# Kernel tuning notes

Hardware: AMD Instinct MI355X
Metric: run time of the kernel (lower is better)

The kernel has to match this reference:

```python
import jax, jax.numpy as jnp
import numpy as np

N = 50000      # nodes
E = 800000     # edges (avg degree 16)
F_IN = 256     # num_node_features
H = 256        # hidden_dim
L = 2          # num_message_passing_rounds - 1 hidden conv layers


def setup_inputs() -> dict:
    key = jax.random.key(0)
    ks = jax.random.split(key, 8)
    x = jax.random.normal(ks[0], (N, F_IN), dtype=jnp.float32)
    edge_index = jax.random.randint(ks[1], (2, E), 0, N, dtype=jnp.int32)
    init = lambda k, shape, fan: jax.random.normal(k, shape, dtype=jnp.float32) / np.float32(np.sqrt(fan))
    WA_in = init(ks[2], (F_IN, H), F_IN)   # proj_in.A weight (stored [in,out])
    WB_in = init(ks[3], (F_IN, H), F_IN)   # proj_in.B weight
    A_stack = init(ks[4], (L, H, H), H)    # conv layers' A weights
    B_stack = init(ks[5], (L, H, H), H)    # conv layers' B weights
    W_out = init(ks[6], (H, 1), H)         # proj_out weight
    b_out = jnp.zeros((1,), jnp.float32)   # proj_out bias
    return {"x": x, "edge_index": edge_index, "WA_in": WA_in, "WB_in": WB_in,
            "A_stack": A_stack, "B_stack": B_stack, "W_out": W_out, "b_out": b_out}


def reference(x, edge_index, WA_in, WB_in, A_stack, B_stack, W_out, b_out):
    src, dst = edge_index[0], edge_index[1]
    # in-degree per node; PyG scatter-mean divides by max(deg, 1)
    deg = jax.ops.segment_sum(jnp.ones((E,), x.dtype), dst, num_segments=N)
    inv_deg = (1.0 / jnp.maximum(deg, 1.0))[:, None]  # [N,1]

    def mean_agg(h):
        # gather x_j = h[src], scatter-mean into dst -> [N, d]
        return jax.ops.segment_sum(h[src], dst, num_segments=N) * inv_deg

    # proj_in: A(mean_msg) + B(x)
    h = mean_agg(x) @ WA_in + x @ WB_in
    # hidden conv rounds with sigmoid (use_relu=False)
    for i in range(L):
        h = jax.nn.sigmoid(mean_agg(h) @ A_stack[i] + h @ B_stack[i])
    # proj_out + squeeze (output_logits=True)
    return (h @ W_out + b_out).squeeze()  # [N]
```

## Files before the change

### kernel.cpp

```cpp
#include <hip/hip_runtime.h>

typedef unsigned short u16;
typedef unsigned int u32;
typedef __attribute__((ext_vector_type(8))) short short8;
typedef __attribute__((ext_vector_type(4))) float f32x4;
typedef __attribute__((ext_vector_type(2))) float f32x2;

__device__ __forceinline__ float bf2f(u16 u) {
    return __uint_as_float(((u32)u) << 16);
}
__device__ __forceinline__ u16 f2bf(float f) {
    u32 u = __float_as_uint(f);
    u += 0x7fff + ((u >> 16) & 1);
    return (u16)(u >> 16);
}
__device__ __forceinline__ u32 pack2(float a, float b) {
    return (u32)f2bf(a) | ((u32)f2bf(b) << 16);
}
__device__ __forceinline__ u32 pk_fp8x4(float f0, float f1, float f2, float f3) {
    int w = __builtin_amdgcn_cvt_pk_fp8_f32(f0, f1, 0, false);
    w = __builtin_amdgcn_cvt_pk_fp8_f32(f2, f3, w, true);
    return (u32)w;
}
__device__ __forceinline__ void acc4(float* a, u32 w) {
    f32x2 lo = __builtin_amdgcn_cvt_pk_f32_fp8((int)w, false);
    f32x2 hi = __builtin_amdgcn_cvt_pk_f32_fp8((int)w, true);
    a[0] += lo.x; a[1] += lo.y; a[2] += hi.x; a[3] += hi.y;
}
__device__ __forceinline__ void acc4m(float* a, u32 w, float m) {
    f32x2 lo = __builtin_amdgcn_cvt_pk_f32_fp8((int)w, false);
    f32x2 hi = __builtin_amdgcn_cvt_pk_f32_fp8((int)w, true);
    a[0] += m * lo.x; a[1] += m * lo.y; a[2] += m * hi.x; a[3] += m * hi.y;
}
__device__ __forceinline__ void acc16(float* a, uint4 v) {
    acc4(a + 0, v.x); acc4(a + 4, v.y); acc4(a + 8, v.z); acc4(a + 12, v.w);
}
__device__ __forceinline__ void acc16m(float* a, uint4 v, float m) {
    acc4m(a + 0, v.x, m); acc4m(a + 4, v.y, m); acc4m(a + 8, v.z, m); acc4m(a + 12, v.w, m);
}


__global__ void cvt_x_kernel(const float* __restrict__ x, u16* __restrict__ xb,
                             u32* __restrict__ xq, int n) {
    int i = blockIdx.x * 256 + threadIdx.x;
    int row = i >> 6;
    ushort4 o;
    u32 q;
    if (row < n) {
        float4 v = ((const float4*)x)[i];
        o.x = f2bf(v.x); o.y = f2bf(v.y); o.z = f2bf(v.z); o.w = f2bf(v.w);
        q = pk_fp8x4(v.x, v.y, v.z, v.w);
    } else {
        o.x = o.y = o.z = o.w = 0;
        q = 0;
    }
    ((ushort4*)xb)[i] = o;
    xq[i] = q;
}

__global__ void cvt_h_kernel(const u16* __restrict__ hb, uint2* __restrict__ hq, int ngroups) {
    int j = blockIdx.x * 256 + threadIdx.x;
    if (j >= ngroups) return;
    uint4 v = ((const uint4*)hb)[j];
    float f0 = bf2f(v.x & 0xffff), f1 = bf2f(v.x >> 16);
    float f2 = bf2f(v.y & 0xffff), f3 = bf2f(v.y >> 16);
    float f4 = bf2f(v.z & 0xffff), f5 = bf2f(v.z >> 16);
    float f6 = bf2f(v.w & 0xffff), f7 = bf2f(v.w >> 16);
    uint2 o;
    o.x = pk_fp8x4(f0, f1, f2, f3);
    o.y = pk_fp8x4(f4, f5, f6, f7);
    hq[j] = o;
}

__global__ void cvt_w_kernel(const float* __restrict__ WA, const float* __restrict__ WB,
                             const float* __restrict__ As, const float* __restrict__ Bs,
                             u16* __restrict__ wT, int nlayers) {
    int i = blockIdx.x * 256 + threadIdx.x;
    const int per = 256 * 512;
    if (i >= nlayers * per) return;
    int l = i / per;
    int rem = i - l * per;
    int nn = rem >> 9;
    int k = rem & 511;
    const float* Aw = (l == 0) ? WA : As + (size_t)(l - 1) * 65536;
    const float* Bw = (l == 0) ? WB : Bs + (size_t)(l - 1) * 65536;
    float v = (k < 256) ? Aw[(size_t)k * 256 + nn] : Bw[(size_t)(k - 256) * 256 + nn];
    wT[i] = f2bf(v);
}


__global__ __launch_bounds__(256) void hist_kernel(const int* __restrict__ dst,
                                                   int* __restrict__ ccnt, int e, int nb) {
    __shared__ int h[256];
    int tid = threadIdx.x;
    h[tid] = 0;
    __syncthreads();
    int e0 = blockIdx.x * 4096;
#pragma unroll
    for (int j = 0; j < 16; ++j) {
        int i = e0 + j * 256 + tid;
        if (i < e) atomicAdd(&h[dst[i] >> 8], 1);
    }
    __syncthreads();
    if (tid < nb) {
        int v = h[tid];
        if (v) atomicAdd(&ccnt[tid], v);
    }
}

__global__ __launch_bounds__(256) void scan_coarse_kernel(const int* __restrict__ ccnt,
                                                          int* __restrict__ cbase,
                                                          int* __restrict__ rowptr,
                                                          int nb, int n, int e) {
    __shared__ int sh[256];
    int t = threadIdx.x;
    int v = (t < nb) ? ccnt[t] : 0;
    int x = v;
    sh[t] = x; __syncthreads();
    for (int o = 1; o < 256; o <<= 1) {
        int y = (t >= o) ? sh[t - o] : 0;
        __syncthreads();
        x += y; sh[t] = x; __syncthreads();
    }
    if (t < nb) cbase[t] = x - v;
    if (t == 0) { cbase[nb] = e; rowptr[n] = e; }
}

__global__ __launch_bounds__(256) void passA_kernel(const int* __restrict__ src,
                                                    const int* __restrict__ dst,
                                                    const int* __restrict__ cbase,
                                                    int* __restrict__ cfill,
                                                    u32* __restrict__ tmp, int e, int nb) {
    __shared__ int ph[256], pb[256], pr[256], cb[256];
    __shared__ u32 ed[4096];
    int tid = threadIdx.x;
    ph[tid] = 0; pr[tid] = 0;
    cb[tid] = (tid < nb) ? cbase[tid] : 0;
    __syncthreads();
    int e0 = blockIdx.x * 4096;
#pragma unroll
    for (int j = 0; j < 16; ++j) {
        int i = e0 + j * 256 + tid;
        u32 p = 0xFFFFFFFFu;
        if (i < e) {
            int d = dst[i];
            p = ((u32)d << 16) | (u32)src[i];
            atomicAdd(&ph[d >> 8], 1);
        }
        ed[j * 256 + tid] = p;
    }
    __syncthreads();
    pb[tid] = (tid < nb && ph[tid]) ? atomicAdd(&cfill[tid], ph[tid]) : 0;
    __syncthreads();
#pragma unroll
    for (int j = 0; j < 16; ++j) {
        u32 p = ed[j * 256 + tid];
        if (p != 0xFFFFFFFFu) {
            int bk = p >> 24;
            int r = atomicAdd(&pr[bk], 1);
            tmp[cb[bk] + pb[bk] + r] = p;
        }
    }
}

__global__ __launch_bounds__(256) void passB_kernel(const u32* __restrict__ tmp,
                                                    const int* __restrict__ cbase,
                                                    int* __restrict__ rowptr,
                                                    float* __restrict__ invd,
                                                    int* __restrict__ srcs, int n) {
    __shared__ int h[256], loc[256], cnt2[256], sh[256];
    int b = blockIdx.x;
    int tid = threadIdx.x;
    int base = cbase[b];
    int cnt = cbase[b + 1] - base;
    int node0 = b << 8;
    h[tid] = 0; cnt2[tid] = 0;
    __syncthreads();
    for (int i = tid; i < cnt; i += 256)
        atomicAdd(&h[(tmp[base + i] >> 16) & 255], 1);
    __syncthreads();
    int c = h[tid];
    int x = c;
    sh[tid] = x; __syncthreads();
    for (int o = 1; o < 256; o <<= 1) {
        int y = (tid >= o) ? sh[tid - o] : 0;
        __syncthreads();
        x += y; sh[tid] = x; __syncthreads();
    }
    loc[tid] = x - c;
    int node = node0 + tid;
    if (node < n) {
        rowptr[node] = base + x - c;
        invd[node] = 1.0f / (float)(c > 0 ? c : 1);
    }
    __syncthreads();
    for (int i = tid; i < cnt; i += 256) {
        u32 p = tmp[base + i];
        int ln = (p >> 16) & 255;
        int r = atomicAdd(&cnt2[ln], 1);
        srcs[base + loc[ln] + r] = (int)(p & 0xffffu);
    }
}


__global__ __launch_bounds__(256) void agg_kernel(const unsigned char* __restrict__ q,
                                                  u16* __restrict__ mb,
                                                  const int* __restrict__ rowptr,
                                                  const int* __restrict__ srcs,
                                                  const float* __restrict__ invd,
                                                  int n, int npad) {
    int gw = (blockIdx.x * 256 + threadIdx.x) >> 6;
    int lane = threadIdx.x & 63;
    int qd = lane >> 4;
    int fl = lane & 15;
    if (gw >= npad) return;
    u16* orow = mb + (size_t)gw * 256;
    if (gw >= n) {
        if (lane < 16) {
            uint4 z; z.x = z.y = z.z = z.w = 0;
            uint4* p = (uint4*)(orow + lane * 16);
            p[0] = z; p[1] = z;
        }
        return;
    }
    int beg = rowptr[gw], end = rowptr[gw + 1];
    float a[16];
#pragma unroll
    for (int i = 0; i < 16; ++i) a[i] = 0.f;
    for (int base = beg; base < end; base += 64) {
        int cnt = end - base;
        if (cnt > 64) cnt = 64;
        int el = (lane < cnt) ? srcs[base + lane] : 0;
        int t = 0;
        for (; 4 * t + 8 <= cnt; t += 2) {
            int s0 = __shfl(el, 4 * t + qd);
            int s1 = __shfl(el, 4 * t + 4 + qd);
            uint4 v0 = *(const uint4*)(q + (size_t)s0 * 256 + fl * 16);
            uint4 v1 = *(const uint4*)(q + (size_t)s1 * 256 + fl * 16);
            acc16(a, v0);
            acc16(a, v1);
        }
        for (; 4 * t < cnt; ++t) {
            int ei = 4 * t + qd;
            int sj = __shfl(el, ei & 63);
            float m = (ei < cnt) ? 1.0f : 0.0f;
            uint4 v = *(const uint4*)(q + (size_t)sj * 256 + fl * 16);
            acc16m(a, v, m);
        }
    }
#pragma unroll
    for (int i = 0; i < 16; ++i) {
        a[i] += __shfl_xor(a[i], 16);
        a[i] += __shfl_xor(a[i], 32);
    }
    if (lane < 16) {
        float sc = invd[gw];
        uint4 o0, o1;
        o0.x = pack2(a[0] * sc, a[1] * sc);
        o0.y = pack2(a[2] * sc, a[3] * sc);
        o0.z = pack2(a[4] * sc, a[5] * sc);
        o0.w = pack2(a[6] * sc, a[7] * sc);
        o1.x = pack2(a[8] * sc, a[9] * sc);
        o1.y = pack2(a[10] * sc, a[11] * sc);
        o1.z = pack2(a[12] * sc, a[13] * sc);
        o1.w = pack2(a[14] * sc, a[15] * sc);
        uint4* p = (uint4*)(orow + lane * 16);
        p[0] = o0; p[1] = o1;
    }
}


__global__ __launch_bounds__(256) void gemm_kernel(const u16* __restrict__ mA,
                                                   const u16* __restrict__ cur,
                                                   const u16* __restrict__ wT,
                                                   u16* __restrict__ outb,
                                                   const float* __restrict__ wo,
                                                   const float* __restrict__ bo,
                                                   float* __restrict__ out,
                                                   int n, int apply_sigmoid, int fin) {
    __shared__ u16 lA[2][64 * 32];
    __shared__ u16 lB[2][256 * 32];
    __shared__ float lO[4][64];
    int r0 = blockIdx.x * 64;
    int tid = threadIdx.x;
    int lane = tid & 63;
    int w = tid >> 6;
    int lrow = lane & 15, quad = lane >> 4;

    f32x4 acc[4][4] = {};

    auto stage = [&](int ks, int b) {
        int k0 = ks * 32;
        const u16* sA = (k0 < 256) ? mA : cur;
        int kk = k0 & 255;
        {
            int li = tid;
            int row = li >> 2;
            int ls = ((li & 3) - row) & 3;
            const u16* g = sA + (size_t)(r0 + row) * 256 + kk + ls * 8;
            __builtin_amdgcn_global_load_lds(
                (const __attribute__((address_space(1))) u32*)g,
                (__attribute__((address_space(3))) u32*)(&lA[b][(size_t)li * 8]), 16, 0, 0);
        }
#pragma unroll
        for (int p = 0; p < 4; ++p) {
            int li = p * 256 + tid;
            int row = li >> 2;
            int ls = ((li & 3) - row) & 3;
            const u16* g = wT + (size_t)row * 512 + k0 + ls * 8;
            __builtin_amdgcn_global_load_lds(
                (const __attribute__((address_space(1))) u32*)g,
                (__attribute__((address_space(3))) u32*)(&lB[b][(size_t)li * 8]), 16, 0, 0);
        }
    };

    stage(0, 0);
    int buf = 0;
    for (int ks = 0; ks < 16; ++ks) {
        __syncthreads();
        if (ks < 15) stage(ks + 1, buf ^ 1);
        short8 a[4], b4[4];
#pragma unroll
        for (int rt = 0; rt < 4; ++rt) {
            int row = rt * 16 + lrow;
            int ps = (quad + row) & 3;
            a[rt] = *(const short8*)(&lA[buf][(size_t)row * 32 + ps * 8]);
        }
#pragma unroll
        for (int ct = 0; ct < 4; ++ct) {
            int row = w * 64 + ct * 16 + lrow;
            int ps = (quad + row) & 3;
            b4[ct] = *(const short8*)(&lB[buf][(size_t)row * 32 + ps * 8]);
        }
#pragma unroll
        for (int rt = 0; rt < 4; ++rt)
#pragma unroll
            for (int ct = 0; ct < 4; ++ct)
                acc[rt][ct] = __builtin_amdgcn_mfma_f32_16x16x32_bf16(a[rt], b4[ct], acc[rt][ct], 0, 0, 0);
        buf ^= 1;
    }

    if (!fin) {
#pragma unroll
        for (int rt = 0; rt < 4; ++rt) {
            int rbase = r0 + rt * 16 + quad * 4;
#pragma unroll
            for (int r = 0; r < 4; ++r) {
                int row = rbase + r;
                if (row < n) {
#pragma unroll
                    for (int ct = 0; ct < 4; ++ct) {
                        float v = acc[rt][ct][r];
                        if (apply_sigmoid) v = 1.0f / (1.0f + __expf(-v));
                        outb[(size_t)row * 256 + w * 64 + ct * 16 + lrow] = f2bf(v);
                    }
                }
            }
        }
    } else {
        float wv[4];
#pragma unroll
        for (int ct = 0; ct < 4; ++ct) wv[ct] = wo[w * 64 + ct * 16 + lrow];
#pragma unroll
        for (int rt = 0; rt < 4; ++rt) {
#pragma unroll
            for (int r = 0; r < 4; ++r) {
                float s = 0.f;
#pragma unroll
                for (int ct = 0; ct < 4; ++ct) {
                    float v = acc[rt][ct][r];
                    v = 1.0f / (1.0f + __expf(-v));
                    s += v * wv[ct];
                }
                s += __shfl_xor(s, 1);
                s += __shfl_xor(s, 2);
                s += __shfl_xor(s, 4);
                s += __shfl_xor(s, 8);
                if (lrow == 0) lO[w][rt * 16 + quad * 4 + r] = s;
            }
        }
        __syncthreads();
        if (tid < 64) {
            int row = r0 + tid;
            if (row < n) out[row] = lO[0][tid] + lO[1][tid] + lO[2][tid] + lO[3][tid] + bo[0];
        }
    }
}


extern "C" void kernel_launch(void* const* d_in, const int* in_sizes, int n_in,
                              void* d_out, int out_size, void* d_ws, size_t ws_size,
                              hipStream_t stream) {
    const float* x  = (const float*)d_in[0];
    const int*   ei = (const int*)d_in[1];
    const float* WA = (const float*)d_in[2];
    const float* WB = (const float*)d_in[3];
    const float* As = (const float*)d_in[4];
    const float* Bs = (const float*)d_in[5];
    const float* Wo = (const float*)d_in[6];
    const float* bo = (const float*)d_in[7];
    float* out = (float*)d_out;

    const int H = 256;
    int N = in_sizes[0] / H;
    int E = in_sizes[1] / 2;
    int L = in_sizes[4] / (H * H);
    int NPAD = (N + 127) & ~127;
    int NB = (N + 255) >> 8;

    char* wsp = (char*)d_ws;
    size_t off = 0;
    auto alloc = [&](size_t b) { size_t o = off; off += (b + 255) & ~(size_t)255; return o; };
    int*   rowptr = (int*)(wsp + alloc((size_t)(NPAD + 1) * 4));
    int*   ccnt   = (int*)(wsp + alloc(1024));
    int*   cbase  = (int*)(wsp + alloc(1032 + 256));
    int*   cfill  = (int*)(wsp + alloc(1024));
    float* invd   = (float*)(wsp + alloc((size_t)NPAD * 4));
    int*   srcs   = (int*)(wsp + alloc((size_t)E * 4));
    u16*   xb     = (u16*)(wsp + alloc((size_t)NPAD * H * 2));
    u16*   hbuf   = (u16*)(wsp + alloc((size_t)NPAD * H * 2));
    u16*   mb     = (u16*)(wsp + alloc((size_t)NPAD * H * 2));
    u32*   xq     = (u32*)(wsp + alloc((size_t)NPAD * H));
    uint2* hq     = (uint2*)(wsp + alloc((size_t)NPAD * H));
    u16*   wT     = (u16*)(wsp + alloc((size_t)(L + 1) * 512 * 256 * 2));
    u32*   tmp    = (u32*)mb;

    const int* esrc = ei;
    const int* edst = ei + E;

    hipMemsetAsync(ccnt, 0, 1024, stream);
    hipMemsetAsync(cfill, 0, 1024, stream);

    int gridE = (E + 4095) / 4096;
    cvt_x_kernel<<<NPAD / 4, 256, 0, stream>>>(x, xb, xq, N);
    cvt_w_kernel<<<((L + 1) * 512 * 256 + 255) / 256, 256, 0, stream>>>(WA, WB, As, Bs, wT, L + 1);
    hist_kernel<<<gridE, 256, 0, stream>>>(edst, ccnt, E, NB);
    scan_coarse_kernel<<<1, 256, 0, stream>>>(ccnt, cbase, rowptr, NB, N, E);
    passA_kernel<<<gridE, 256, 0, stream>>>(esrc, edst, cbase, cfill, tmp, E, NB);
    passB_kernel<<<NB, 256, 0, stream>>>(tmp, cbase, rowptr, invd, srcs, N);

    const u16* cur = xb;
    const unsigned char* curq = (const unsigned char*)xq;
    for (int s = 0; s <= L; ++s) {
        int fin = (s == L) ? 1 : 0;
        agg_kernel<<<NPAD / 4, 256, 0, stream>>>(curq, mb, rowptr, srcs, invd, N, NPAD);
        gemm_kernel<<<NPAD / 64, 256, 0, stream>>>(mb, cur, wT + (size_t)s * 512 * 256, hbuf,
                                                   Wo, bo, out, N, s > 0 ? 1 : 0, fin);
        if (!fin) {
            cvt_h_kernel<<<(N * 32 + 255) / 256, 256, 0, stream>>>(hbuf, hq, N * 32);
            cur = hbuf;
            curq = (const unsigned char*)hq;
        }
    }
}
```

Measured before the change: 365.0 us.

## Make GEMM persistent with LDS-resident weight quarter per block

```diff
diff --git a/kernel.cpp b/kernel.cpp
--- a/kernel.cpp
+++ b/kernel.cpp
@@ -1,5 +1,6 @@
 #include <hip/hip_runtime.h>
 
+typedef unsigned char u8;
 typedef unsigned short u16;
 typedef unsigned int u32;
 typedef __attribute__((ext_vector_type(8))) short short8;
@@ -203,7 +204,7 @@
 }
 
 
-__global__ __launch_bounds__(256) void agg_kernel(const unsigned char* __restrict__ q,
+__global__ __launch_bounds__(256) void agg_kernel(const u8* __restrict__ q,
                                                   u16* __restrict__ mb,
                                                   const int* __restrict__ rowptr,
                                                   const int* __restrict__ srcs,
@@ -270,105 +271,77 @@
 }
 
 
-__global__ __launch_bounds__(256) void gemm_kernel(const u16* __restrict__ mA,
-                                                   const u16* __restrict__ cur,
-                                                   const u16* __restrict__ wT,
-                                                   u16* __restrict__ outb,
-                                                   const float* __restrict__ wo,
-                                                   const float* __restrict__ bo,
-                                                   float* __restrict__ out,
-                                                   int n, int apply_sigmoid, int fin) {
-    __shared__ u16 lA[2][64 * 32];
-    __shared__ u16 lB[2][256 * 32];
-    __shared__ float lO[4][64];
-    int r0 = blockIdx.x * 64;
+__global__ __launch_bounds__(512, 4) void gemm_kernel(const u16* __restrict__ mb,
+                                                      const u16* __restrict__ cur,
+                                                      const u16* __restrict__ wT,
+                                                      u16* __restrict__ hout,
+                                                      const float* __restrict__ wo,
+                                                      const float* __restrict__ bo,
+                                                      float* __restrict__ out,
+                                                      int n, int ntiles, int sig, int fin) {
+    __shared__ u16 lB[64 * 512];
     int tid = threadIdx.x;
+    int bid = blockIdx.x;
+    int qtr = bid & 3;
+    int w = tid >> 6;
     int lane = tid & 63;
-    int w = tid >> 6;
     int lrow = lane & 15, quad = lane >> 4;
-
-    f32x4 acc[4][4] = {};
-
-    auto stage = [&](int ks, int b) {
-        int k0 = ks * 32;
-        const u16* sA = (k0 < 256) ? mA : cur;
-        int kk = k0 & 255;
-        {
-            int li = tid;
-            int row = li >> 2;
-            int ls = ((li & 3) - row) & 3;
-            const u16* g = sA + (size_t)(r0 + row) * 256 + kk + ls * 8;
-            __builtin_amdgcn_global_load_lds(
-                (const __attribute__((address_space(1))) u32*)g,
-                (__attribute__((address_space(3))) u32*)(&lA[b][(size_t)li * 8]), 16, 0, 0);
-        }
-#pragma unroll
-        for (int p = 0; p < 4; ++p) {
-            int li = p * 256 + tid;
-            int row = li >> 2;
-            int ls = ((li & 3) - row) & 3;
-            const u16* g = wT + (size_t)row * 512 + k0 + ls * 8;
-            __builtin_amdgcn_global_load_lds(
-                (const __attribute__((address_space(1))) u32*)g,
-                (__attribute__((address_space(3))) u32*)(&lB[b][(size_t)li * 8]), 16, 0, 0);
-        }
-    };
-
-    stage(0, 0);
-    int buf = 0;
-    for (int ks = 0; ks < 16; ++ks) {
-        __syncthreads();
-        if (ks < 15) stage(ks + 1, buf ^ 1);
-        short8 a[4], b4[4];
-#pragma unroll
-        for (int rt = 0; rt < 4; ++rt) {
-            int row = rt * 16 + lrow;
-            int ps = (quad + row) & 3;
-            a[rt] = *(const short8*)(&lA[buf][(size_t)row * 32 + ps * 8]);
-        }
-#pragma unroll
-        for (int ct = 0; ct < 4; ++ct) {
-            int row = w * 64 + ct * 16 + lrow;
-            int ps = (quad + row) & 3;
-            b4[ct] = *(const short8*)(&lB[buf][(size_t)row * 32 + ps * 8]);
-        }
-#pragma unroll
-        for (int rt = 0; rt < 4; ++rt)
-#pragma unroll
-            for (int ct = 0; ct < 4; ++ct)
-                acc[rt][ct] = __builtin_amdgcn_mfma_f32_16x16x32_bf16(a[rt], b4[ct], acc[rt][ct], 0, 0, 0);
-        buf ^= 1;
-    }
-
-    if (!fin) {
-#pragma unroll
-        for (int rt = 0; rt < 4; ++rt) {
-            int rbase = r0 + rt * 16 + quad * 4;
-#pragma unroll
-            for (int r = 0; r < 4; ++r) {
-                int row = rbase + r;
-                if (row < n) {
-#pragma unroll
-                    for (int ct = 0; ct < 4; ++ct) {
-                        float v = acc[rt][ct][r];
-                        if (apply_sigmoid) v = 1.0f / (1.0f + __expf(-v));
-                        outb[(size_t)row * 256 + w * 64 + ct * 16 + lrow] = f2bf(v);
-                    }
+    int wslot = (bid >> 2) * 8 + w;
+    int wstride = (gridDim.x >> 2) * 8;
+
+    const u16* wsrc = wT + (size_t)qtr * 64 * 512;
+#pragma unroll
+    for (int i = tid; i < 64 * 64; i += 512) {
+        int nn = i >> 6, s = i & 63;
+        uint4 v = *(const uint4*)(wsrc + (size_t)nn * 512 + s * 8);
+        *(uint4*)((u8*)lB + (size_t)nn * 1024 + ((s ^ nn) << 4)) = v;
+    }
+    __syncthreads();
+
+    float bo0 = bo[0];
+    for (int t = wslot; t < ntiles; t += wstride) {
+        int r0 = t * 16;
+        const u16* am = mb + (size_t)(r0 + lrow) * 256 + quad * 8;
+        const u16* ac = cur + (size_t)(r0 + lrow) * 256 + quad * 8;
+        short8 av[16];
+#pragma unroll
+        for (int ks = 0; ks < 8; ++ks) av[ks] = *(const short8*)(am + ks * 32);
+#pragma unroll
+        for (int ks = 0; ks < 8; ++ks) av[8 + ks] = *(const short8*)(ac + ks * 32);
+
+        f32x4 acc[4] = {};
+#pragma unroll
+        for (int ks = 0; ks < 16; ++ks) {
+#pragma unroll
+            for (int ct = 0; ct < 4; ++ct) {
+                int nn = ct * 16 + lrow;
+                int slot = ks * 4 + quad;
+                short8 b = *(const short8*)((const u8*)lB + (size_t)nn * 1024 + ((slot ^ nn) << 4));
+                acc[ct] = __builtin_amdgcn_mfma_f32_16x16x32_bf16(av[ks], b, acc[ct], 0, 0, 0);
+            }
+        }
+
+        if (!fin) {
+#pragma unroll
+            for (int ct = 0; ct < 4; ++ct) {
+#pragma unroll
+                for (int r = 0; r < 4; ++r) {
+                    float v = acc[ct][r];
+                    if (sig) v = 1.0f / (1.0f + __expf(-v));
+                    int row = r0 + quad * 4 + r;
+                    hout[(size_t)row * 256 + qtr * 64 + ct * 16 + lrow] = f2bf(v);
                 }
             }
-        }
-    } else {
-        float wv[4];
-#pragma unroll
-        for (int ct = 0; ct < 4; ++ct) wv[ct] = wo[w * 64 + ct * 16 + lrow];
-#pragma unroll
-        for (int rt = 0; rt < 4; ++rt) {
+        } else {
+            float wv[4];
+#pragma unroll
+            for (int ct = 0; ct < 4; ++ct) wv[ct] = wo[qtr * 64 + ct * 16 + lrow];
 #pragma unroll
             for (int r = 0; r < 4; ++r) {
                 float s = 0.f;
 #pragma unroll
                 for (int ct = 0; ct < 4; ++ct) {
-                    float v = acc[rt][ct][r];
+                    float v = acc[ct][r];
                     v = 1.0f / (1.0f + __expf(-v));
                     s += v * wv[ct];
                 }
@@ -376,13 +349,11 @@
                 s += __shfl_xor(s, 2);
                 s += __shfl_xor(s, 4);
                 s += __shfl_xor(s, 8);
-                if (lrow == 0) lO[w][rt * 16 + quad * 4 + r] = s;
+                if (lrow == 0) {
+                    int row = r0 + quad * 4 + r;
+                    if (row < n) atomicAdd(&out[row], s + (qtr == 0 ? bo0 : 0.f));
+                }
             }
-        }
-        __syncthreads();
-        if (tid < 64) {
-            int row = r0 + tid;
-            if (row < n) out[row] = lO[0][tid] + lO[1][tid] + lO[2][tid] + lO[3][tid] + bo[0];
         }
     }
 }
@@ -407,6 +378,7 @@
     int L = in_sizes[4] / (H * H);
     int NPAD = (N + 127) & ~127;
     int NB = (N + 255) >> 8;
+    int ntiles = NPAD / 16;
 
     char* wsp = (char*)d_ws;
     size_t off = 0;
@@ -418,10 +390,11 @@
     float* invd   = (float*)(wsp + alloc((size_t)NPAD * 4));
     int*   srcs   = (int*)(wsp + alloc((size_t)E * 4));
     u16*   xb     = (u16*)(wsp + alloc((size_t)NPAD * H * 2));
-    u16*   hbuf   = (u16*)(wsp + alloc((size_t)NPAD * H * 2));
+    u16*   h0     = (u16*)(wsp + alloc((size_t)NPAD * H * 2));
+    u16*   h1     = (u16*)(wsp + alloc((size_t)NPAD * H * 2));
     u16*   mb     = (u16*)(wsp + alloc((size_t)NPAD * H * 2));
-    u32*   xq     = (u32*)(wsp + alloc((size_t)NPAD * H));
-    uint2* hq     = (uint2*)(wsp + alloc((size_t)NPAD * H));
+    u8*    xq     = (u8*)(wsp + alloc((size_t)NPAD * H));
+    u8*    hq     = (u8*)(wsp + alloc((size_t)NPAD * H));
     u16*   wT     = (u16*)(wsp + alloc((size_t)(L + 1) * 512 * 256 * 2));
     u32*   tmp    = (u32*)mb;
 
@@ -430,9 +403,10 @@
 
     hipMemsetAsync(ccnt, 0, 1024, stream);
     hipMemsetAsync(cfill, 0, 1024, stream);
+    hipMemsetAsync(out, 0, (size_t)N * 4, stream);
 
     int gridE = (E + 4095) / 4096;
-    cvt_x_kernel<<<NPAD / 4, 256, 0, stream>>>(x, xb, xq, N);
+    cvt_x_kernel<<<NPAD / 4, 256, 0, stream>>>(x, xb, (u32*)xq, N);
     cvt_w_kernel<<<((L + 1) * 512 * 256 + 255) / 256, 256, 0, stream>>>(WA, WB, As, Bs, wT, L + 1);
     hist_kernel<<<gridE, 256, 0, stream>>>(edst, ccnt, E, NB);
     scan_coarse_kernel<<<1, 256, 0, stream>>>(ccnt, cbase, rowptr, NB, N, E);
@@ -440,16 +414,17 @@
     passB_kernel<<<NB, 256, 0, stream>>>(tmp, cbase, rowptr, invd, srcs, N);
 
     const u16* cur = xb;
-    const unsigned char* curq = (const unsigned char*)xq;
+    const u8*  curq = xq;
     for (int s = 0; s <= L; ++s) {
         int fin = (s == L) ? 1 : 0;
+        u16* nxt = (s & 1) ? h1 : h0;
         agg_kernel<<<NPAD / 4, 256, 0, stream>>>(curq, mb, rowptr, srcs, invd, N, NPAD);
-        gemm_kernel<<<NPAD / 64, 256, 0, stream>>>(mb, cur, wT + (size_t)s * 512 * 256, hbuf,
-                                                   Wo, bo, out, N, s > 0 ? 1 : 0, fin);
+        gemm_kernel<<<512, 512, 0, stream>>>(mb, cur, wT + (size_t)s * 512 * 256, nxt,
+                                             Wo, bo, out, N, ntiles, s > 0 ? 1 : 0, fin);
         if (!fin) {
-            cvt_h_kernel<<<(N * 32 + 255) / 256, 256, 0, stream>>>(hbuf, hq, N * 32);
-            cur = hbuf;
-            curq = (const unsigned char*)hq;
-        }
-    }
-}
+            cvt_h_kernel<<<(N * 32 + 255) / 256, 256, 0, stream>>>(nxt, (uint2*)hq, N * 32);
+            cur = nxt;
+            curq = hq;
+        }
+    }
+}
```

New measurement: 764.3 us. +109.4%, slower.
